# Kernel tuning notes

Hardware: AMD Instinct MI355X
Metric: run time of the kernel (lower is better)

The kernel has to match this reference:

```python
import jax, jax.numpy as jnp
import numpy as np

N = 100000       # nodes
E = 1000000      # edges
IN = 128         # in_dim
HID = 64         # hid_dim
NET = 4          # n_etypes
STEPS = 5        # n_steps
G = 128          # graphs in batch
LBL = 10         # num_labels


def setup_inputs() -> dict:
    key = jax.random.key(0)
    ks = jax.random.split(key, 20)
    def w(k, shape, fan_in):
        return jax.random.normal(k, shape, jnp.float32) / np.sqrt(fan_in)
    return dict(
        x=jax.random.normal(ks[0], (N, IN), jnp.float32),
        src=jax.random.randint(ks[1], (E,), 0, N),
        dst=jax.random.randint(ks[2], (E,), 0, N),
        etype=jax.random.randint(ks[3], (E,), 0, NET),
        node2graph=jnp.sort(jax.random.randint(ks[4], (N,), 0, G)),
        # linear_in
        W_in=w(ks[5], (HID, IN), IN), b_in=jnp.zeros((HID,), jnp.float32),
        # per-edge-type linears [n_etypes, out, in]
        We=w(ks[6], (NET, HID, HID), HID), be=jnp.zeros((NET, HID), jnp.float32),
        # GRUCell (torch layout: rows = [r; z; n])
        W_ih=w(ks[7], (3 * HID, HID), HID), b_ih=jnp.zeros((3 * HID,), jnp.float32),
        W_hh=w(ks[8], (3 * HID, HID), HID), b_hh=jnp.zeros((3 * HID,), jnp.float32),
        # classifier
        W1=w(ks[9], (HID // 2, HID), HID), b1=jnp.zeros((HID // 2,), jnp.float32),
        W2=w(ks[10], (LBL, HID // 2), HID // 2), b2=jnp.zeros((LBL,), jnp.float32),
    )


def reference(x, W_in, b_in, We, be, W_ih, b_ih, W_hh, b_hh, W1, b1, W2, b2,
              src, dst, etype, node2graph):
    h = x @ W_in.T + b_in                                  # [N, HID]
    for _ in range(STEPS):
        # per-etype linear on node states: trans[e] = h @ We[e].T + be[e]
        trans = jnp.einsum('nd,efd->enf', h, We) + be[:, None, :]  # [NET, N, HID]
        msgs = trans[etype, src]                           # [E, HID] gather per edge
        a = jax.ops.segment_sum(msgs, dst, num_segments=N)  # scatter-add aggregation
        # GRUCell(a, h)
        gi = a @ W_ih.T + b_ih
        gh = h @ W_hh.T + b_hh
        ir, iz, i_n = jnp.split(gi, 3, axis=-1)
        hr, hz, h_n = jnp.split(gh, 3, axis=-1)
        r = jax.nn.sigmoid(ir + hr)
        z = jax.nn.sigmoid(iz + hz)
        n = jnp.tanh(i_n + r * h_n)
        h = (1.0 - z) * n + z * h
    # dgl.mean_nodes: per-graph mean of node states
    cnt = jnp.maximum(jax.ops.segment_sum(jnp.ones((N,), h.dtype), node2graph, num_segments=G), 1.0)
    hg = jax.ops.segment_sum(h, node2graph, num_segments=G) / cnt[:, None]  # [G, HID]
    return jax.nn.relu(hg @ W1.T + b1) @ W2.T + b2         # [G, LBL]
```

## Files before the change

kernel.cpp:

```cpp
#include <hip/hip_runtime.h>
#include <hip/hip_bf16.h>
#include <math.h>

#define N_NODES 100000
#define N_EDGES 1000000
#define IN_DIM 128
#define HID 64
#define NET 4
#define STEPS 5
#define G_GRAPHS 128
#define LBL 10
#define NGRP 6250
#define NGRP_PAD 6256
#define NBKT 1024
#define TILE_E 8192

typedef __attribute__((ext_vector_type(8))) short short8;
typedef __attribute__((ext_vector_type(4))) float f32x4;
typedef unsigned short ushort_t;

__device__ inline ushort_t f2bf(float v) {
    __hip_bfloat16 b = __float2bfloat16(v);
    return __builtin_bit_cast(ushort_t, b);
}
__device__ inline float bf2f(ushort_t u) {
    __hip_bfloat16 b = __builtin_bit_cast(__hip_bfloat16, u);
    return __bfloat162float(b);
}


__global__ void k_pack_bc(const float* __restrict__ We, ushort_t* __restrict__ BC) {
    int idx = blockIdx.x * blockDim.x + threadIdx.x;
    if (idx >= 24 * 4 * 64 * 8) return;
    int j = idx & 7, lane = (idx >> 3) & 63, ct = (idx >> 9) & 3, sl = idx >> 11;
    int g = lane >> 4, u = lane & 15;
    int p = sl >> 3, ks = sl & 7;
    int k = ks * 32 + g * 8 + j;
    int t = k >> 6, d = k & 63;
    int o = ct * 16 + u;
    float val = We[t * 4096 + o * 64 + d];
    ushort_t hi = f2bf(val);
    BC[idx] = (p < 2) ? hi : f2bf(val - bf2f(hi));
}

__global__ void k_pack_b2(const float* __restrict__ W_ih, const float* __restrict__ b_ih,
                          const float* __restrict__ W_hh, const float* __restrict__ b_hh,
                          ushort_t* __restrict__ B2, float* __restrict__ bg2) {
    int idx = blockIdx.x * blockDim.x + threadIdx.x;
    if (idx >= 12 * 16 * 4 * 16 * 8) return;
    int j = idx & 7, u = (idx >> 3) & 15, g = (idx >> 7) & 3, ct = (idx >> 9) & 15, s = idx >> 13;
    int m = ct * 16 + u;
    int q = m >> 6, gate = (m >> 4) & 3, c = q * 16 + (m & 15);
    int k = (s & 3) * 32 + g * 8 + j;
    float val;
    if (gate == 0)      { int jr = c;        val = (k < 64) ? W_ih[jr * 64 + k] : W_hh[jr * 64 + k - 64]; }
    else if (gate == 1) { int jr = 64 + c;   val = (k < 64) ? W_ih[jr * 64 + k] : W_hh[jr * 64 + k - 64]; }
    else if (gate == 2) { int jr = 128 + c;  val = (k < 64) ? W_ih[jr * 64 + k] : 0.f; }
    else                { int jr = 128 + c;  val = (k < 64) ? 0.f : W_hh[jr * 64 + k - 64]; }
    ushort_t hi = f2bf(val);
    B2[idx] = (s < 8) ? hi : f2bf(val - bf2f(hi));
    if (s == 0 && g == 0 && j == 0) {
        float bv;
        if (gate == 0)      bv = b_ih[c] + b_hh[c];
        else if (gate == 1) bv = b_ih[64 + c] + b_hh[64 + c];
        else if (gate == 2) bv = b_ih[128 + c];
        else                bv = b_hh[128 + c];
        bg2[m] = bv;
    }
}

__global__ void k_pack_bin(const float* __restrict__ W_in, ushort_t* __restrict__ BIN) {
    int idx = blockIdx.x * blockDim.x + threadIdx.x;
    if (idx >= 24576) return;
    int j = idx & 7, lu = (idx >> 3) & 63, ct = (idx >> 9) & 3, s = idx >> 11;
    int g = lu >> 4, u = lu & 15;
    int m = ct * 16 + u;
    int k = (s & 3) * 32 + g * 8 + j;
    float val = W_in[m * 128 + k];
    ushort_t hi = f2bf(val);
    BIN[idx] = (s < 8) ? hi : f2bf(val - bf2f(hi));
}

__global__ __launch_bounds__(256) void k_linear_in(const float* __restrict__ x,
        const ushort_t* __restrict__ BIN, const float* __restrict__ b_in,
        ushort_t* __restrict__ AH, ushort_t* __restrict__ hrow) {
    __shared__ float hlds[4][16 * 68];
    int tid = threadIdx.x;
    int lane = tid & 63, wp = tid >> 6;
    int g = lane >> 4, u = lane & 15;
    int grp = blockIdx.x * 4 + wp;
    bool ok = grp < NGRP;
    int row = ok ? (grp * 16 + u) : 0;
    short8 xhi[4], xlo[4];
    #pragma unroll
    for (int ks = 0; ks < 4; ++ks) {
        const float* xp = &x[(size_t)row * 128 + ks * 32 + g * 8];
        float4 v0 = ok ? *(const float4*)xp : make_float4(0.f, 0.f, 0.f, 0.f);
        float4 v1 = ok ? *(const float4*)(xp + 4) : make_float4(0.f, 0.f, 0.f, 0.f);
        float vv[8] = {v0.x, v0.y, v0.z, v0.w, v1.x, v1.y, v1.z, v1.w};
        #pragma unroll
        for (int j = 0; j < 8; ++j) {
            ushort_t hh = f2bf(vv[j]);
            xhi[ks][j] = (short)hh;
            xlo[ks][j] = (short)f2bf(vv[j] - bf2f(hh));
        }
    }
    f32x4 zero = {0.f, 0.f, 0.f, 0.f};
    f32x4 acc[4] = {zero, zero, zero, zero};
    #pragma unroll
    for (int s = 0; s < 12; ++s) {
        int ks = s & 3;
        short8 af = (s < 4) ? xhi[ks] : (s < 8) ? xlo[ks] : xhi[ks];
        #pragma unroll
        for (int ct = 0; ct < 4; ++ct) {
            short8 bf = *(const short8*)&BIN[((size_t)(s * 4 + ct) * 64 + lane) * 8];
            acc[ct] = __builtin_amdgcn_mfma_f32_16x16x32_bf16(af, bf, acc[ct], 0, 0, 0);
        }
    }
    #pragma unroll
    for (int ct = 0; ct < 4; ++ct) {
        float bo = b_in[ct * 16 + u];
        #pragma unroll
        for (int j = 0; j < 4; ++j)
            hlds[wp][(g * 4 + j) * 68 + ct * 16 + u] = acc[ct][j] + bo;
    }
    __syncthreads();
    #pragma unroll
    for (int k = 0; k < 4; ++k) {
        int bi = g + 4 * k;
        short8 ov;
        #pragma unroll
        for (int j = 0; j < 8; ++j) {
            float v = hlds[wp][u * 68 + (bi & 7) * 8 + j];
            ushort_t hh = f2bf(v);
            ov[j] = (bi < 8) ? (short)hh : (short)f2bf(v - bf2f(hh));
        }
        int blk = (bi < 8) ? (8 + bi) : (24 + (bi - 8));
        if (ok) {
            *(short8*)&AH[((size_t)grp * 32 + blk) * 128 + u * 8] = ov;
            if (bi < 8)
                *(short8*)&hrow[((size_t)(grp * 16 + u)) * 64 + bi * 8] = ov;
        }
    }
}

__global__ __launch_bounds__(256) void k_bhist(const int* __restrict__ dst,
        int* __restrict__ bhist) {
    __shared__ int h[NBKT];
    for (int i = threadIdx.x; i < NBKT; i += 256) h[i] = 0;
    __syncthreads();
    int idx = blockIdx.x * 256 + threadIdx.x;
    for (int e = idx; e < N_EDGES; e += 256 * 256) atomicAdd(&h[dst[e] >> 7], 1);
    __syncthreads();
    for (int i = threadIdx.x; i < NBKT; i += 256) {
        int c = h[i];
        if (c) atomicAdd(&bhist[i], c);
    }
}

__global__ __launch_bounds__(1024) void k_bscan(const int* __restrict__ bhist,
        int* __restrict__ bbase, int* __restrict__ bcursor) {
    __shared__ int ts[NBKT];
    int t = threadIdx.x;
    int v = bhist[t];
    ts[t] = v;
    __syncthreads();
    for (int off = 1; off < NBKT; off <<= 1) {
        int u = (t >= off) ? ts[t - off] : 0;
        __syncthreads();
        ts[t] += u;
        __syncthreads();
    }
    int excl = ts[t] - v;
    bbase[t] = excl;
    bcursor[t] = excl;
    if (t == NBKT - 1) bbase[NBKT] = ts[NBKT - 1];
}

__global__ __launch_bounds__(512) void k_bscatter(const int* __restrict__ src,
        const int* __restrict__ dst, const int* __restrict__ et,
        int* __restrict__ bcursor, unsigned int* __restrict__ ebuf) {
    __shared__ int hcnt[NBKT], loff[NBKT], gpos[NBKT], ps[512];
    __shared__ unsigned int stage[TILE_E];
    __shared__ unsigned short sbkt[TILE_E];
    int tid = threadIdx.x;
    int base = blockIdx.x * TILE_E;
    int tilecnt = min(TILE_E, N_EDGES - base);
    for (int i = tid; i < NBKT; i += 512) hcnt[i] = 0;
    __syncthreads();
    #pragma unroll
    for (int k = 0; k < TILE_E / 512; ++k) {
        int e = base + tid + k * 512;
        if (e < N_EDGES) atomicAdd(&hcnt[dst[e] >> 7], 1);
    }
    __syncthreads();
    int c0 = hcnt[tid * 2], c1 = hcnt[tid * 2 + 1];
    ps[tid] = c0 + c1;
    __syncthreads();
    for (int off = 1; off < 512; off <<= 1) {
        int u = (tid >= off) ? ps[tid - off] : 0;
        __syncthreads();
        ps[tid] += u;
        __syncthreads();
    }
    int ex = ps[tid] - (c0 + c1);
    loff[tid * 2] = ex;
    loff[tid * 2 + 1] = ex + c0;
    for (int b = tid; b < NBKT; b += 512) {
        int c = hcnt[b];
        gpos[b] = c ? atomicAdd(&bcursor[b], c) : 0;
    }
    __syncthreads();
    for (int i = tid; i < NBKT; i += 512) hcnt[i] = 0;
    __syncthreads();
    #pragma unroll
    for (int k = 0; k < TILE_E / 512; ++k) {
        int e = base + tid + k * 512;
        if (e < N_EDGES) {
            int d = dst[e];
            int b = d >> 7;
            int r = atomicAdd(&hcnt[b], 1);
            int lp = loff[b] + r;
            stage[lp] = (unsigned int)src[e] | ((unsigned int)et[e] << 20)
                      | ((unsigned int)(d & 127) << 22);
            sbkt[lp] = (unsigned short)b;
        }
    }
    __syncthreads();
    for (int i = tid; i < tilecnt; i += 512) {
        int b = sbkt[i];
        ebuf[gpos[b] + (i - loff[b])] = stage[i];
    }
}

__global__ __launch_bounds__(256) void k_bcsr(const unsigned int* __restrict__ ebuf,
        const int* __restrict__ bbase, int* __restrict__ adj, int* __restrict__ row_ptr) {
    __shared__ int ncnt[128], noff[129], nps[128];
    int b = blockIdx.x;
    int tid = threadIdx.x;
    int ebeg = bbase[b], eend = bbase[b + 1];
    int ecnt = eend - ebeg;
    if (tid < 128) ncnt[tid] = 0;
    __syncthreads();
    for (int i = tid; i < ecnt; i += 256) atomicAdd(&ncnt[(ebuf[ebeg + i] >> 22) & 127], 1);
    __syncthreads();
    int v = (tid < 128) ? ncnt[tid] : 0;
    if (tid < 128) nps[tid] = v;
    __syncthreads();
    for (int off = 1; off < 128; off <<= 1) {
        int u = (tid >= off && tid < 128) ? nps[tid - off] : 0;
        __syncthreads();
        if (tid < 128) nps[tid] += u;
        __syncthreads();
    }
    if (tid < 128) noff[tid] = nps[tid] - v;
    if (tid == 127) noff[128] = nps[127];
    __syncthreads();
    if (tid < 128) ncnt[tid] = 0;
    __syncthreads();
    for (int i = tid; i < ecnt; i += 256) {
        unsigned int p = ebuf[ebeg + i];
        int nl = (p >> 22) & 127;
        int r = atomicAdd(&ncnt[nl], 1);
        adj[ebeg + noff[nl] + r] = (int)(p & 0x3FFFFF);
    }
    for (int i = tid; i <= 128; i += 256) {
        int n = b * 128 + i;
        if (n <= N_NODES) row_ptr[n] = ebeg + noff[i];
    }
}

__global__ __launch_bounds__(512) void k_step(const int* __restrict__ row_ptr,
        const int* __restrict__ adj, const ushort_t* __restrict__ hin,
        ushort_t* __restrict__ hout, ushort_t* __restrict__ AH,
        const ushort_t* __restrict__ BC, const float* __restrict__ be,
        const ushort_t* __restrict__ B2, const float* __restrict__ bg2) {
    __shared__ float smem[16896];
    float* aggf = smem;
    float* cnts = smem + 16640;
    ushort_t* als  = (ushort_t*)smem;
    ushort_t* hlds = (ushort_t*)((char*)smem + 17408);

    int tid = threadIdx.x, lane = tid & 63, wp = tid >> 6;
    int g = lane >> 4, u = lane & 15;
    int grp0 = blockIdx.x * 4;
    int nbase = grp0 * 16;

    #pragma unroll 1
    for (int r = 0; r < 8; ++r) {
        int nl = wp * 8 + r;
        int n = nbase + nl;
        float a0 = 0.f, a1 = 0.f, a2 = 0.f, a3 = 0.f;
        float c0 = 0.f, c1 = 0.f, c2 = 0.f, c3 = 0.f;
        if (n < N_NODES) {
            int beg = row_ptr[n], end = row_ptr[n + 1];
            int i = beg;
            for (; i + 4 <= end; i += 4) {
                int p0 = adj[i], p1 = adj[i + 1], p2 = adj[i + 2], p3 = adj[i + 3];
                float v0 = bf2f(hin[(size_t)(p0 & 0xFFFFF) * 64 + lane]);
                float v1 = bf2f(hin[(size_t)(p1 & 0xFFFFF) * 64 + lane]);
                float v2 = bf2f(hin[(size_t)(p2 & 0xFFFFF) * 64 + lane]);
                float v3 = bf2f(hin[(size_t)(p3 & 0xFFFFF) * 64 + lane]);
                int e0 = p0 >> 20, e1 = p1 >> 20, e2 = p2 >> 20, e3 = p3 >> 20;
                a0 += (e0 == 0) ? v0 : 0.f; a1 += (e0 == 1) ? v0 : 0.f;
                a2 += (e0 == 2) ? v0 : 0.f; a3 += (e0 == 3) ? v0 : 0.f;
                a0 += (e1 == 0) ? v1 : 0.f; a1 += (e1 == 1) ? v1 : 0.f;
                a2 += (e1 == 2) ? v1 : 0.f; a3 += (e1 == 3) ? v1 : 0.f;
                a0 += (e2 == 0) ? v2 : 0.f; a1 += (e2 == 1) ? v2 : 0.f;
                a2 += (e2 == 2) ? v2 : 0.f; a3 += (e2 == 3) ? v2 : 0.f;
                a0 += (e3 == 0) ? v3 : 0.f; a1 += (e3 == 1) ? v3 : 0.f;
                a2 += (e3 == 2) ? v3 : 0.f; a3 += (e3 == 3) ? v3 : 0.f;
                c0 += ((e0 == 0) ? 1.f : 0.f) + ((e1 == 0) ? 1.f : 0.f) + ((e2 == 0) ? 1.f : 0.f) + ((e3 == 0) ? 1.f : 0.f);
                c1 += ((e0 == 1) ? 1.f : 0.f) + ((e1 == 1) ? 1.f : 0.f) + ((e2 == 1) ? 1.f : 0.f) + ((e3 == 1) ? 1.f : 0.f);
                c2 += ((e0 == 2) ? 1.f : 0.f) + ((e1 == 2) ? 1.f : 0.f) + ((e2 == 2) ? 1.f : 0.f) + ((e3 == 2) ? 1.f : 0.f);
                c3 += ((e0 == 3) ? 1.f : 0.f) + ((e1 == 3) ? 1.f : 0.f) + ((e2 == 3) ? 1.f : 0.f) + ((e3 == 3) ? 1.f : 0.f);
            }
            for (; i < end; ++i) {
                int pk = adj[i];
                float v = bf2f(hin[(size_t)(pk & 0xFFFFF) * 64 + lane]);
                int e = pk >> 20;
                a0 += (e == 0) ? v : 0.f; a1 += (e == 1) ? v : 0.f;
                a2 += (e == 2) ? v : 0.f; a3 += (e == 3) ? v : 0.f;
                c0 += (e == 0) ? 1.f : 0.f; c1 += (e == 1) ? 1.f : 0.f;
                c2 += (e == 2) ? 1.f : 0.f; c3 += (e == 3) ? 1.f : 0.f;
            }
        }
        aggf[nl * 260 +   0 + lane] = a0;
        aggf[nl * 260 +  64 + lane] = a1;
        aggf[nl * 260 + 128 + lane] = a2;
        aggf[nl * 260 + 192 + lane] = a3;
        if (lane == 0) {
            cnts[nl * 4 + 0] = c0; cnts[nl * 4 + 1] = c1;
            cnts[nl * 4 + 2] = c2; cnts[nl * 4 + 3] = c3;
        }
    }
    __syncthreads();

    int rp1 = wp >> 1, cq = wp & 1;
    f32x4 zero = {0.f, 0.f, 0.f, 0.f};
    f32x4 acc1[2] = {zero, zero};
    #pragma unroll
    for (int ks = 0; ks < 8; ++ks) {
        const float* ap = &aggf[(rp1 * 16 + u) * 260 + ks * 32 + g * 8];
        f32x4 x0 = *(const f32x4*)ap;
        f32x4 x1 = *(const f32x4*)(ap + 4);
        short8 ahi, alo;
        #pragma unroll
        for (int j = 0; j < 4; ++j) {
            ushort_t hh = f2bf(x0[j]);
            ahi[j] = (short)hh; alo[j] = (short)f2bf(x0[j] - bf2f(hh));
            ushort_t hh2 = f2bf(x1[j]);
            ahi[4 + j] = (short)hh2; alo[4 + j] = (short)f2bf(x1[j] - bf2f(hh2));
        }
        #pragma unroll
        for (int p = 0; p < 3; ++p) {
            short8 af = (p == 1) ? alo : ahi;
            #pragma unroll
            for (int ct = 0; ct < 2; ++ct) {
                short8 bf = *(const short8*)&BC[((size_t)((p * 8 + ks) * 4 + cq * 2 + ct) * 64 + lane) * 8];
                acc1[ct] = __builtin_amdgcn_mfma_f32_16x16x32_bf16(af, bf, acc1[ct], 0, 0, 0);
            }
        }
    }
    __syncthreads();

    {
        float beL[2][4];
        #pragma unroll
        for (int ct = 0; ct < 2; ++ct)
            #pragma unroll
            for (int t = 0; t < 4; ++t)
                beL[ct][t] = be[t * 64 + cq * 32 + ct * 16 + u];
        #pragma unroll
        for (int j = 0; j < 4; ++j) {
            int row = rp1 * 16 + g * 4 + j;
            f32x4 cn = *(const f32x4*)&cnts[row * 4];
            #pragma unroll
            for (int ct = 0; ct < 2; ++ct) {
                float v = acc1[ct][j] + cn[0] * beL[ct][0] + cn[1] * beL[ct][1]
                                      + cn[2] * beL[ct][2] + cn[3] * beL[ct][3];
                int col = cq * 32 + ct * 16 + u;
                ushort_t hh = f2bf(v);
                als[row * 136 + col] = hh;
                als[row * 136 + 64 + col] = f2bf(v - bf2f(hh));
            }
        }
    }
    #pragma unroll
    for (int it = 0; it < 2; ++it) {
        int c = it * 512 + tid;
        int gl = c >> 8, r = c & 255, bi = r >> 4, uu = r & 15;
        int blk = (bi < 8) ? (8 + bi) : (24 + (bi - 8));
        *(short8*)&hlds[((gl * 16 + bi) * 16 + uu) * 8] =
            *(const short8*)&AH[((size_t)(grp0 + gl) * 32 + blk) * 128 + uu * 8];
    }
    __syncthreads();

    int q = wp & 3, rp2 = wp >> 2;
    f32x4 acc2[2][4];
    #pragma unroll
    for (int i = 0; i < 2; ++i)
        #pragma unroll
        for (int j = 0; j < 4; ++j) acc2[i][j] = zero;
    #pragma unroll
    for (int s = 0; s < 12; ++s) {
        int p2 = s >> 2, ks2 = s & 3;
        short8 bfr[4], afr[2];
        #pragma unroll
        for (int ct = 0; ct < 4; ++ct)
            bfr[ct] = *(const short8*)&B2[((size_t)(s * 16 + q * 4 + ct) * 64 + g * 16 + u) * 8];
        #pragma unroll
        for (int rt = 0; rt < 2; ++rt) {
            int row = rp2 * 32 + rt * 16 + u;
            if (ks2 < 2) {
                int base = ((p2 == 1) ? 64 : 0) + ks2 * 32 + g * 8;
                afr[rt] = *(const short8*)&als[row * 136 + base];
            } else {
                int part = (p2 == 1) ? 1 : 0;
                int gl = rp2 * 2 + rt;
                int bi = part * 8 + (ks2 - 2) * 4 + g;
                afr[rt] = *(const short8*)&hlds[((gl * 16 + bi) * 16 + u) * 8];
            }
        }
        #pragma unroll
        for (int rt = 0; rt < 2; ++rt)
            #pragma unroll
            for (int ct = 0; ct < 4; ++ct)
                acc2[rt][ct] = __builtin_amdgcn_mfma_f32_16x16x32_bf16(afr[rt], bfr[ct], acc2[rt][ct], 0, 0, 0);
    }
    __syncthreads();

    {
        float bgv[4];
        #pragma unroll
        for (int ct = 0; ct < 4; ++ct) bgv[ct] = bg2[q * 64 + ct * 16 + u];
        int hid = q * 16 + u;
        #pragma unroll
        for (int rt = 0; rt < 2; ++rt) {
            int gl = rp2 * 2 + rt;
            #pragma unroll
            for (int j = 0; j < 4; ++j) {
                int uu = g * 4 + j;
                int shi = ((gl * 16 + (hid >> 3)) * 16 + uu) * 8 + (hid & 7);
                int slo = ((gl * 16 + 8 + (hid >> 3)) * 16 + uu) * 8 + (hid & 7);
                float ho = bf2f(hlds[shi]) + bf2f(hlds[slo]);
                float rs  = acc2[rt][0][j] + bgv[0];
                float zs  = acc2[rt][1][j] + bgv[1];
                float inn = acc2[rt][2][j] + bgv[2];
                float hnn = acc2[rt][3][j] + bgv[3];
                float rr = 1.f / (1.f + __expf(-rs));
                float zz = 1.f / (1.f + __expf(-zs));
                float t = inn + rr * hnn;
                float e2 = __expf(2.f * t);
                float nn = 1.f - 2.f / (e2 + 1.f);
                float hnew = (1.f - zz) * nn + zz * ho;
                ushort_t hh = f2bf(hnew);
                hlds[shi] = hh;
                hlds[slo] = f2bf(hnew - bf2f(hh));
            }
        }
    }
    __syncthreads();

    #pragma unroll
    for (int it = 0; it < 2; ++it) {
        int c = it * 512 + tid;
        int gl = c >> 8, r = c & 255, bi = r >> 4, uu = r & 15;
        short8 v = *(const short8*)&hlds[((gl * 16 + bi) * 16 + uu) * 8];
        int blk = (bi < 8) ? (8 + bi) : (24 + (bi - 8));
        *(short8*)&AH[((size_t)(grp0 + gl) * 32 + blk) * 128 + uu * 8] = v;
        if (bi < 8)
            *(short8*)&hout[((size_t)((grp0 + gl) * 16 + uu)) * 64 + bi * 8] = v;
    }
}

__global__ __launch_bounds__(256) void k_pool(const int* __restrict__ n2g,
        const ushort_t* __restrict__ AH, float* __restrict__ hg) {
    int gidx = blockIdx.x;
    int lo = 0, hi = N_NODES;
    while (lo < hi) { int mid = (lo + hi) >> 1; if (n2g[mid] < gidx) lo = mid + 1; else hi = mid; }
    int s = lo;
    hi = N_NODES;
    while (lo < hi) { int mid = (lo + hi) >> 1; if (n2g[mid] < gidx + 1) lo = mid + 1; else hi = mid; }
    int e = lo;
    int w = threadIdx.x >> 6, lane = threadIdx.x & 63;
    int bh = 8 + (lane >> 3), bl = 24 + (lane >> 3), el = lane & 7;
    float sum = 0.f;
    for (int n = s + w; n < e; n += 4) {
        size_t base = (size_t)(n >> 4) * 4096 + (size_t)(n & 15) * 8;
        sum += bf2f(AH[base + bh * 128 + el]) + bf2f(AH[base + bl * 128 + el]);
    }
    __shared__ float red[4][64];
    red[w][lane] = sum;
    __syncthreads();
    if (threadIdx.x < 64) {
        float tot = red[0][lane] + red[1][lane] + red[2][lane] + red[3][lane];
        float cnt = (float)(e - s);
        hg[gidx * 64 + lane] = tot / fmaxf(cnt, 1.f);
    }
}

__global__ __launch_bounds__(64) void k_cls(const float* __restrict__ hg,
        const float* __restrict__ W1, const float* __restrict__ b1,
        const float* __restrict__ W2, const float* __restrict__ b2,
        float* __restrict__ out) {
    int gidx = blockIdx.x;
    __shared__ float v[64];
    __shared__ float m[32];
    v[threadIdx.x] = hg[gidx * 64 + threadIdx.x];
    __syncthreads();
    if (threadIdx.x < 32) {
        float a = b1[threadIdx.x];
        #pragma unroll 8
        for (int k = 0; k < 64; ++k) a = fmaf(v[k], W1[threadIdx.x * 64 + k], a);
        m[threadIdx.x] = fmaxf(a, 0.f);
    }
    __syncthreads();
    if (threadIdx.x < 10) {
        float a = b2[threadIdx.x];
        #pragma unroll
        for (int j = 0; j < 32; ++j) a = fmaf(m[j], W2[threadIdx.x * 32 + j], a);
        out[gidx * 10 + threadIdx.x] = a;
    }
}

extern "C" void kernel_launch(void* const* d_in, const int* in_sizes, int n_in,
                              void* d_out, int out_size, void* d_ws, size_t ws_size,
                              hipStream_t stream) {
    const float* x    = (const float*)d_in[0];
    const int* src    = (const int*)d_in[1];
    const int* dst    = (const int*)d_in[2];
    const int* etype  = (const int*)d_in[3];
    const int* n2g    = (const int*)d_in[4];
    const float* W_in = (const float*)d_in[5];
    const float* b_in = (const float*)d_in[6];
    const float* We   = (const float*)d_in[7];
    const float* be   = (const float*)d_in[8];
    const float* W_ih = (const float*)d_in[9];
    const float* b_ih = (const float*)d_in[10];
    const float* W_hh = (const float*)d_in[11];
    const float* b_hh = (const float*)d_in[12];
    const float* W1   = (const float*)d_in[13];
    const float* b1   = (const float*)d_in[14];
    const float* W2   = (const float*)d_in[15];
    const float* b2   = (const float*)d_in[16];
    float* out = (float*)d_out;

    char* wsb = (char*)d_ws;
    size_t off = 0;
    auto alloc = [&](size_t bytes) -> void* {
        void* p = wsb + off;
        off += (bytes + 255) & ~(size_t)255;
        return p;
    };
    ushort_t* AH      = (ushort_t*)alloc((size_t)NGRP_PAD * 4096 * 2);
    ushort_t* hrowA   = (ushort_t*)alloc((size_t)NGRP_PAD * 16 * 64 * 2);
    ushort_t* hrowB   = (ushort_t*)alloc((size_t)NGRP_PAD * 16 * 64 * 2);
    int*      adj     = (int*)     alloc((size_t)N_EDGES * 4);
    unsigned int* ebuf = (unsigned int*)alloc((size_t)N_EDGES * 4);
    int*      row_ptr = (int*)     alloc((size_t)(N_NODES + 1) * 4);
    int*      bhist   = (int*)     alloc((size_t)NBKT * 4);
    int*      bbase   = (int*)     alloc((size_t)(NBKT + 1) * 4);
    int*      bcursor = (int*)     alloc((size_t)NBKT * 4);
    ushort_t* B2      = (ushort_t*)alloc((size_t)12 * 16 * 4 * 16 * 8 * 2);
    float*    bg2     = (float*)   alloc(256 * 4);
    ushort_t* BIN     = (ushort_t*)alloc((size_t)24576 * 2);
    ushort_t* BC      = (ushort_t*)alloc((size_t)24 * 4 * 64 * 8 * 2);
    float*    hg      = (float*)   alloc(128 * 64 * 4);

    hipMemsetAsync(AH + (size_t)NGRP * 4096, 0, (size_t)(NGRP_PAD - NGRP) * 4096 * 2, stream);

    hipLaunchKernelGGL(k_pack_b2, dim3(384), dim3(256), 0, stream, W_ih, b_ih, W_hh, b_hh, B2, bg2);
    hipLaunchKernelGGL(k_pack_bin, dim3(96), dim3(256), 0, stream, W_in, BIN);
    hipLaunchKernelGGL(k_pack_bc, dim3(192), dim3(256), 0, stream, We, BC);
    hipLaunchKernelGGL(k_linear_in, dim3((NGRP + 3) / 4), dim3(256), 0, stream, x, BIN, b_in, AH, hrowA);

    hipMemsetAsync(bhist, 0, (size_t)NBKT * 4, stream);
    hipLaunchKernelGGL(k_bhist, dim3(256), dim3(256), 0, stream, dst, bhist);
    hipLaunchKernelGGL(k_bscan, dim3(1), dim3(1024), 0, stream, bhist, bbase, bcursor);
    hipLaunchKernelGGL(k_bscatter, dim3((N_EDGES + TILE_E - 1) / TILE_E), dim3(512), 0, stream,
                       src, dst, etype, bcursor, ebuf);
    hipLaunchKernelGGL(k_bcsr, dim3(NBKT), dim3(256), 0, stream, ebuf, bbase, adj, row_ptr);

    int sblk = NGRP_PAD / 4;
    for (int step = 0; step < STEPS; ++step) {
        const ushort_t* hin = (step & 1) ? hrowB : hrowA;
        ushort_t* hout      = (step & 1) ? hrowA : hrowB;
        hipLaunchKernelGGL(k_step, dim3(sblk), dim3(512), 0, stream,
                           row_ptr, adj, hin, hout, AH, BC, be, B2, bg2);
    }
    hipLaunchKernelGGL(k_pool, dim3(G_GRAPHS), dim3(256), 0, stream, n2g, AH, hg);
    hipLaunchKernelGGL(k_cls, dim3(G_GRAPHS), dim3(64), 0, stream, hg, W1, b1, W2, b2, out);
}
```

Before: 841.4 us.

## Sort CSR edges by (dst, etype) and halve k_step tile to 32 nodes

The CSR build now buckets edges by destination node and edge type, producing a four-way row pointer per node. The gather loop can then sum each edge-type segment directly, with no per-edge select over four accumulators, and counts come from pointer differences. Separately, each k_step block now handles 32 nodes instead of 64, halving shared memory and doubling the block count for more occupancy, at the cost of fewer MFMAs per B-fragment load. The padded buffers and the memset are removed because 6250 groups divide evenly by 2.

```diff
diff --git a/kernel.cpp b/kernel.cpp
--- a/kernel.cpp
+++ b/kernel.cpp
@@ -11,7 +11,6 @@
 #define G_GRAPHS 128
 #define LBL 10
 #define NGRP 6250
-#define NGRP_PAD 6256
 #define NBKT 1024
 #define TILE_E 8192
 
@@ -234,111 +233,97 @@
 }
 
 __global__ __launch_bounds__(256) void k_bcsr(const unsigned int* __restrict__ ebuf,
-        const int* __restrict__ bbase, int* __restrict__ adj, int* __restrict__ row_ptr) {
-    __shared__ int ncnt[128], noff[129], nps[128];
+        const int* __restrict__ bbase, int* __restrict__ adj, int* __restrict__ row_ptr2) {
+    __shared__ int ncnt[512], noff[513], ps[256];
     int b = blockIdx.x;
     int tid = threadIdx.x;
     int ebeg = bbase[b], eend = bbase[b + 1];
     int ecnt = eend - ebeg;
-    if (tid < 128) ncnt[tid] = 0;
-    __syncthreads();
-    for (int i = tid; i < ecnt; i += 256) atomicAdd(&ncnt[(ebuf[ebeg + i] >> 22) & 127], 1);
-    __syncthreads();
-    int v = (tid < 128) ? ncnt[tid] : 0;
-    if (tid < 128) nps[tid] = v;
-    __syncthreads();
-    for (int off = 1; off < 128; off <<= 1) {
-        int u = (tid >= off && tid < 128) ? nps[tid - off] : 0;
-        __syncthreads();
-        if (tid < 128) nps[tid] += u;
-        __syncthreads();
-    }
-    if (tid < 128) noff[tid] = nps[tid] - v;
-    if (tid == 127) noff[128] = nps[127];
-    __syncthreads();
-    if (tid < 128) ncnt[tid] = 0;
+    ncnt[tid] = 0; ncnt[tid + 256] = 0;
     __syncthreads();
     for (int i = tid; i < ecnt; i += 256) {
         unsigned int p = ebuf[ebeg + i];
-        int nl = (p >> 22) & 127;
-        int r = atomicAdd(&ncnt[nl], 1);
-        adj[ebeg + noff[nl] + r] = (int)(p & 0x3FFFFF);
-    }
-    for (int i = tid; i <= 128; i += 256) {
-        int n = b * 128 + i;
-        if (n <= N_NODES) row_ptr[n] = ebeg + noff[i];
-    }
-}
-
-__global__ __launch_bounds__(512) void k_step(const int* __restrict__ row_ptr,
+        int key = (int)((((p >> 22) & 127) << 2) | ((p >> 20) & 3));
+        atomicAdd(&ncnt[key], 1);
+    }
+    __syncthreads();
+    int c0 = ncnt[2 * tid], c1 = ncnt[2 * tid + 1];
+    ps[tid] = c0 + c1;
+    __syncthreads();
+    for (int off = 1; off < 256; off <<= 1) {
+        int u = (tid >= off) ? ps[tid - off] : 0;
+        __syncthreads();
+        ps[tid] += u;
+        __syncthreads();
+    }
+    int ex = ps[tid] - (c0 + c1);
+    noff[2 * tid] = ex;
+    noff[2 * tid + 1] = ex + c0;
+    if (tid == 255) noff[512] = ps[255];
+    __syncthreads();
+    ncnt[tid] = 0; ncnt[tid + 256] = 0;
+    __syncthreads();
+    for (int i = tid; i < ecnt; i += 256) {
+        unsigned int p = ebuf[ebeg + i];
+        int key = (int)((((p >> 22) & 127) << 2) | ((p >> 20) & 3));
+        int r = atomicAdd(&ncnt[key], 1);
+        adj[ebeg + noff[key] + r] = (int)(p & 0xFFFFF);
+    }
+    for (int k = tid; k < 512; k += 256)
+        row_ptr2[b * 512 + k] = ebeg + noff[k];
+    if (b == NBKT - 1 && tid == 0) row_ptr2[NBKT * 512] = eend;
+}
+
+__global__ __launch_bounds__(512) void k_step(const int* __restrict__ row_ptr2,
         const int* __restrict__ adj, const ushort_t* __restrict__ hin,
         ushort_t* __restrict__ hout, ushort_t* __restrict__ AH,
         const ushort_t* __restrict__ BC, const float* __restrict__ be,
         const ushort_t* __restrict__ B2, const float* __restrict__ bg2) {
-    __shared__ float smem[16896];
+    __shared__ float smem[8448];
     float* aggf = smem;
-    float* cnts = smem + 16640;
+    float* cnts = smem + 8320;
     ushort_t* als  = (ushort_t*)smem;
-    ushort_t* hlds = (ushort_t*)((char*)smem + 17408);
+    ushort_t* hlds = (ushort_t*)((char*)smem + 9216);
 
     int tid = threadIdx.x, lane = tid & 63, wp = tid >> 6;
     int g = lane >> 4, u = lane & 15;
-    int grp0 = blockIdx.x * 4;
+    int grp0 = blockIdx.x * 2;
     int nbase = grp0 * 16;
 
     #pragma unroll 1
-    for (int r = 0; r < 8; ++r) {
-        int nl = wp * 8 + r;
+    for (int r = 0; r < 4; ++r) {
+        int nl = wp * 4 + r;
         int n = nbase + nl;
-        float a0 = 0.f, a1 = 0.f, a2 = 0.f, a3 = 0.f;
-        float c0 = 0.f, c1 = 0.f, c2 = 0.f, c3 = 0.f;
-        if (n < N_NODES) {
-            int beg = row_ptr[n], end = row_ptr[n + 1];
-            int i = beg;
-            for (; i + 4 <= end; i += 4) {
-                int p0 = adj[i], p1 = adj[i + 1], p2 = adj[i + 2], p3 = adj[i + 3];
-                float v0 = bf2f(hin[(size_t)(p0 & 0xFFFFF) * 64 + lane]);
-                float v1 = bf2f(hin[(size_t)(p1 & 0xFFFFF) * 64 + lane]);
-                float v2 = bf2f(hin[(size_t)(p2 & 0xFFFFF) * 64 + lane]);
-                float v3 = bf2f(hin[(size_t)(p3 & 0xFFFFF) * 64 + lane]);
-                int e0 = p0 >> 20, e1 = p1 >> 20, e2 = p2 >> 20, e3 = p3 >> 20;
-                a0 += (e0 == 0) ? v0 : 0.f; a1 += (e0 == 1) ? v0 : 0.f;
-                a2 += (e0 == 2) ? v0 : 0.f; a3 += (e0 == 3) ? v0 : 0.f;
-                a0 += (e1 == 0) ? v1 : 0.f; a1 += (e1 == 1) ? v1 : 0.f;
-                a2 += (e1 == 2) ? v1 : 0.f; a3 += (e1 == 3) ? v1 : 0.f;
-                a0 += (e2 == 0) ? v2 : 0.f; a1 += (e2 == 1) ? v2 : 0.f;
-                a2 += (e2 == 2) ? v2 : 0.f; a3 += (e2 == 3) ? v2 : 0.f;
-                a0 += (e3 == 0) ? v3 : 0.f; a1 += (e3 == 1) ? v3 : 0.f;
-                a2 += (e3 == 2) ? v3 : 0.f; a3 += (e3 == 3) ? v3 : 0.f;
-                c0 += ((e0 == 0) ? 1.f : 0.f) + ((e1 == 0) ? 1.f : 0.f) + ((e2 == 0) ? 1.f : 0.f) + ((e3 == 0) ? 1.f : 0.f);
-                c1 += ((e0 == 1) ? 1.f : 0.f) + ((e1 == 1) ? 1.f : 0.f) + ((e2 == 1) ? 1.f : 0.f) + ((e3 == 1) ? 1.f : 0.f);
-                c2 += ((e0 == 2) ? 1.f : 0.f) + ((e1 == 2) ? 1.f : 0.f) + ((e2 == 2) ? 1.f : 0.f) + ((e3 == 2) ? 1.f : 0.f);
-                c3 += ((e0 == 3) ? 1.f : 0.f) + ((e1 == 3) ? 1.f : 0.f) + ((e2 == 3) ? 1.f : 0.f) + ((e3 == 3) ? 1.f : 0.f);
+        const int* op = &row_ptr2[(size_t)n * 4];
+        int o0 = op[0], o1 = op[1], o2 = op[2], o3 = op[3], o4 = op[4];
+        #pragma unroll
+        for (int t = 0; t < 4; ++t) {
+            int i = (t == 0) ? o0 : (t == 1) ? o1 : (t == 2) ? o2 : o3;
+            int e = (t == 0) ? o1 : (t == 1) ? o2 : (t == 2) ? o3 : o4;
+            float s0 = 0.f, s1 = 0.f, s2 = 0.f, s3 = 0.f;
+            for (; i + 4 <= e; i += 4) {
+                int a0 = adj[i], a1 = adj[i + 1], a2 = adj[i + 2], a3 = adj[i + 3];
+                s0 += bf2f(hin[(size_t)a0 * 64 + lane]);
+                s1 += bf2f(hin[(size_t)a1 * 64 + lane]);
+                s2 += bf2f(hin[(size_t)a2 * 64 + lane]);
+                s3 += bf2f(hin[(size_t)a3 * 64 + lane]);
             }
-            for (; i < end; ++i) {
-                int pk = adj[i];
-                float v = bf2f(hin[(size_t)(pk & 0xFFFFF) * 64 + lane]);
-                int e = pk >> 20;
-                a0 += (e == 0) ? v : 0.f; a1 += (e == 1) ? v : 0.f;
-                a2 += (e == 2) ? v : 0.f; a3 += (e == 3) ? v : 0.f;
-                c0 += (e == 0) ? 1.f : 0.f; c1 += (e == 1) ? 1.f : 0.f;
-                c2 += (e == 2) ? 1.f : 0.f; c3 += (e == 3) ? 1.f : 0.f;
-            }
-        }
-        aggf[nl * 260 +   0 + lane] = a0;
-        aggf[nl * 260 +  64 + lane] = a1;
-        aggf[nl * 260 + 128 + lane] = a2;
-        aggf[nl * 260 + 192 + lane] = a3;
+            for (; i < e; ++i)
+                s0 += bf2f(hin[(size_t)adj[i] * 64 + lane]);
+            aggf[nl * 260 + t * 64 + lane] = (s0 + s1) + (s2 + s3);
+        }
         if (lane == 0) {
-            cnts[nl * 4 + 0] = c0; cnts[nl * 4 + 1] = c1;
-            cnts[nl * 4 + 2] = c2; cnts[nl * 4 + 3] = c3;
-        }
-    }
-    __syncthreads();
-
-    int rp1 = wp >> 1, cq = wp & 1;
+            cnts[nl * 4 + 0] = (float)(o1 - o0);
+            cnts[nl * 4 + 1] = (float)(o2 - o1);
+            cnts[nl * 4 + 2] = (float)(o3 - o2);
+            cnts[nl * 4 + 3] = (float)(o4 - o3);
+        }
+    }
+    __syncthreads();
+
+    int rp1 = wp >> 2, cq = wp & 3;
     f32x4 zero = {0.f, 0.f, 0.f, 0.f};
-    f32x4 acc1[2] = {zero, zero};
+    f32x4 acc1 = zero;
     #pragma unroll
     for (int ks = 0; ks < 8; ++ks) {
         const float* ap = &aggf[(rp1 * 16 + u) * 260 + ks * 32 + g * 8];
@@ -355,41 +340,31 @@
         #pragma unroll
         for (int p = 0; p < 3; ++p) {
             short8 af = (p == 1) ? alo : ahi;
-            #pragma unroll
-            for (int ct = 0; ct < 2; ++ct) {
-                short8 bf = *(const short8*)&BC[((size_t)((p * 8 + ks) * 4 + cq * 2 + ct) * 64 + lane) * 8];
-                acc1[ct] = __builtin_amdgcn_mfma_f32_16x16x32_bf16(af, bf, acc1[ct], 0, 0, 0);
-            }
+            short8 bf = *(const short8*)&BC[((size_t)((p * 8 + ks) * 4 + cq) * 64 + lane) * 8];
+            acc1 = __builtin_amdgcn_mfma_f32_16x16x32_bf16(af, bf, acc1, 0, 0, 0);
         }
     }
     __syncthreads();
 
     {
-        float beL[2][4];
-        #pragma unroll
-        for (int ct = 0; ct < 2; ++ct)
-            #pragma unroll
-            for (int t = 0; t < 4; ++t)
-                beL[ct][t] = be[t * 64 + cq * 32 + ct * 16 + u];
+        float beL[4];
+        #pragma unroll
+        for (int t = 0; t < 4; ++t) beL[t] = be[t * 64 + cq * 16 + u];
         #pragma unroll
         for (int j = 0; j < 4; ++j) {
             int row = rp1 * 16 + g * 4 + j;
             f32x4 cn = *(const f32x4*)&cnts[row * 4];
-            #pragma unroll
-            for (int ct = 0; ct < 2; ++ct) {
-                float v = acc1[ct][j] + cn[0] * beL[ct][0] + cn[1] * beL[ct][1]
-                                      + cn[2] * beL[ct][2] + cn[3] * beL[ct][3];
-                int col = cq * 32 + ct * 16 + u;
-                ushort_t hh = f2bf(v);
-                als[row * 136 + col] = hh;
-                als[row * 136 + 64 + col] = f2bf(v - bf2f(hh));
-            }
-        }
-    }
-    #pragma unroll
-    for (int it = 0; it < 2; ++it) {
-        int c = it * 512 + tid;
-        int gl = c >> 8, r = c & 255, bi = r >> 4, uu = r & 15;
+            float v = acc1[j] + cn[0] * beL[0] + cn[1] * beL[1]
+                              + cn[2] * beL[2] + cn[3] * beL[3];
+            int col = cq * 16 + u;
+            ushort_t hh = f2bf(v);
+            als[row * 136 + col] = hh;
+            als[row * 136 + 64 + col] = f2bf(v - bf2f(hh));
+        }
+    }
+    {
+        int c = tid;
+        int gl = c >> 8, rr = c & 255, bi = rr >> 4, uu = rr & 15;
         int blk = (bi < 8) ? (8 + bi) : (24 + (bi - 8));
         *(short8*)&hlds[((gl * 16 + bi) * 16 + uu) * 8] =
             *(const short8*)&AH[((size_t)(grp0 + gl) * 32 + blk) * 128 + uu * 8];
@@ -397,36 +372,24 @@
     __syncthreads();
 
     int q = wp & 3, rp2 = wp >> 2;
-    f32x4 acc2[2][4];
-    #pragma unroll
-    for (int i = 0; i < 2; ++i)
-        #pragma unroll
-        for (int j = 0; j < 4; ++j) acc2[i][j] = zero;
+    f32x4 acc2[4] = {zero, zero, zero, zero};
     #pragma unroll
     for (int s = 0; s < 12; ++s) {
         int p2 = s >> 2, ks2 = s & 3;
-        short8 bfr[4], afr[2];
-        #pragma unroll
-        for (int ct = 0; ct < 4; ++ct)
-            bfr[ct] = *(const short8*)&B2[((size_t)(s * 16 + q * 4 + ct) * 64 + g * 16 + u) * 8];
-        #pragma unroll
-        for (int rt = 0; rt < 2; ++rt) {
-            int row = rp2 * 32 + rt * 16 + u;
-            if (ks2 < 2) {
-                int base = ((p2 == 1) ? 64 : 0) + ks2 * 32 + g * 8;
-                afr[rt] = *(const short8*)&als[row * 136 + base];
-            } else {
-                int part = (p2 == 1) ? 1 : 0;
-                int gl = rp2 * 2 + rt;
-                int bi = part * 8 + (ks2 - 2) * 4 + g;
-                afr[rt] = *(const short8*)&hlds[((gl * 16 + bi) * 16 + u) * 8];
-            }
-        }
-        #pragma unroll
-        for (int rt = 0; rt < 2; ++rt)
-            #pragma unroll
-            for (int ct = 0; ct < 4; ++ct)
-                acc2[rt][ct] = __builtin_amdgcn_mfma_f32_16x16x32_bf16(afr[rt], bfr[ct], acc2[rt][ct], 0, 0, 0);
+        short8 afr;
+        if (ks2 < 2) {
+            int base = ((p2 == 1) ? 64 : 0) + ks2 * 32 + g * 8;
+            afr = *(const short8*)&als[(rp2 * 16 + u) * 136 + base];
+        } else {
+            int part = (p2 == 1) ? 1 : 0;
+            int bi = part * 8 + (ks2 - 2) * 4 + g;
+            afr = *(const short8*)&hlds[((rp2 * 16 + bi) * 16 + u) * 8];
+        }
+        #pragma unroll
+        for (int ct = 0; ct < 4; ++ct) {
+            short8 bfr = *(const short8*)&B2[((size_t)(s * 16 + q * 4 + ct) * 64 + g * 16 + u) * 8];
+            acc2[ct] = __builtin_amdgcn_mfma_f32_16x16x32_bf16(afr, bfr, acc2[ct], 0, 0, 0);
+        }
     }
     __syncthreads();
 
@@ -436,36 +399,31 @@
         for (int ct = 0; ct < 4; ++ct) bgv[ct] = bg2[q * 64 + ct * 16 + u];
         int hid = q * 16 + u;
         #pragma unroll
-        for (int rt = 0; rt < 2; ++rt) {
-            int gl = rp2 * 2 + rt;
-            #pragma unroll
-            for (int j = 0; j < 4; ++j) {
-                int uu = g * 4 + j;
-                int shi = ((gl * 16 + (hid >> 3)) * 16 + uu) * 8 + (hid & 7);
-                int slo = ((gl * 16 + 8 + (hid >> 3)) * 16 + uu) * 8 + (hid & 7);
-                float ho = bf2f(hlds[shi]) + bf2f(hlds[slo]);
-                float rs  = acc2[rt][0][j] + bgv[0];
-                float zs  = acc2[rt][1][j] + bgv[1];
-                float inn = acc2[rt][2][j] + bgv[2];
-                float hnn = acc2[rt][3][j] + bgv[3];
-                float rr = 1.f / (1.f + __expf(-rs));
-                float zz = 1.f / (1.f + __expf(-zs));
-                float t = inn + rr * hnn;
-                float e2 = __expf(2.f * t);
-                float nn = 1.f - 2.f / (e2 + 1.f);
-                float hnew = (1.f - zz) * nn + zz * ho;
-                ushort_t hh = f2bf(hnew);
-                hlds[shi] = hh;
-                hlds[slo] = f2bf(hnew - bf2f(hh));
-            }
-        }
-    }
-    __syncthreads();
-
-    #pragma unroll
-    for (int it = 0; it < 2; ++it) {
-        int c = it * 512 + tid;
-        int gl = c >> 8, r = c & 255, bi = r >> 4, uu = r & 15;
+        for (int j = 0; j < 4; ++j) {
+            int uu = g * 4 + j;
+            int shi = ((rp2 * 16 + (hid >> 3)) * 16 + uu) * 8 + (hid & 7);
+            int slo = ((rp2 * 16 + 8 + (hid >> 3)) * 16 + uu) * 8 + (hid & 7);
+            float ho = bf2f(hlds[shi]) + bf2f(hlds[slo]);
+            float rs  = acc2[0][j] + bgv[0];
+            float zs  = acc2[1][j] + bgv[1];
+            float inn = acc2[2][j] + bgv[2];
+            float hnn = acc2[3][j] + bgv[3];
+            float rr = 1.f / (1.f + __expf(-rs));
+            float zz = 1.f / (1.f + __expf(-zs));
+            float t = inn + rr * hnn;
+            float e2 = __expf(2.f * t);
+            float nn = 1.f - 2.f / (e2 + 1.f);
+            float hnew = (1.f - zz) * nn + zz * ho;
+            ushort_t hh = f2bf(hnew);
+            hlds[shi] = hh;
+            hlds[slo] = f2bf(hnew - bf2f(hh));
+        }
+    }
+    __syncthreads();
+
+    {
+        int c = tid;
+        int gl = c >> 8, rr = c & 255, bi = rr >> 4, uu = rr & 15;
         short8 v = *(const short8*)&hlds[((gl * 16 + bi) * 16 + uu) * 8];
         int blk = (bi < 8) ? (8 + bi) : (24 + (bi - 8));
         *(short8*)&AH[((size_t)(grp0 + gl) * 32 + blk) * 128 + uu * 8] = v;
@@ -553,22 +511,20 @@
         off += (bytes + 255) & ~(size_t)255;
         return p;
     };
-    ushort_t* AH      = (ushort_t*)alloc((size_t)NGRP_PAD * 4096 * 2);
-    ushort_t* hrowA   = (ushort_t*)alloc((size_t)NGRP_PAD * 16 * 64 * 2);
-    ushort_t* hrowB   = (ushort_t*)alloc((size_t)NGRP_PAD * 16 * 64 * 2);
-    int*      adj     = (int*)     alloc((size_t)N_EDGES * 4);
+    ushort_t* AH       = (ushort_t*)alloc((size_t)NGRP * 4096 * 2);
+    ushort_t* hrowA    = (ushort_t*)alloc((size_t)N_NODES * 64 * 2);
+    ushort_t* hrowB    = (ushort_t*)alloc((size_t)N_NODES * 64 * 2);
+    int*      adj      = (int*)     alloc((size_t)N_EDGES * 4);
     unsigned int* ebuf = (unsigned int*)alloc((size_t)N_EDGES * 4);
-    int*      row_ptr = (int*)     alloc((size_t)(N_NODES + 1) * 4);
-    int*      bhist   = (int*)     alloc((size_t)NBKT * 4);
-    int*      bbase   = (int*)     alloc((size_t)(NBKT + 1) * 4);
-    int*      bcursor = (int*)     alloc((size_t)NBKT * 4);
-    ushort_t* B2      = (ushort_t*)alloc((size_t)12 * 16 * 4 * 16 * 8 * 2);
-    float*    bg2     = (float*)   alloc(256 * 4);
-    ushort_t* BIN     = (ushort_t*)alloc((size_t)24576 * 2);
-    ushort_t* BC      = (ushort_t*)alloc((size_t)24 * 4 * 64 * 8 * 2);
-    float*    hg      = (float*)   alloc(128 * 64 * 4);
-
-    hipMemsetAsync(AH + (size_t)NGRP * 4096, 0, (size_t)(NGRP_PAD - NGRP) * 4096 * 2, stream);
+    int*      row_ptr2 = (int*)     alloc(((size_t)NBKT * 512 + 1) * 4);
+    int*      bhist    = (int*)     alloc((size_t)NBKT * 4);
+    int*      bbase    = (int*)     alloc((size_t)(NBKT + 1) * 4);
+    int*      bcursor  = (int*)     alloc((size_t)NBKT * 4);
+    ushort_t* B2       = (ushort_t*)alloc((size_t)12 * 16 * 4 * 16 * 8 * 2);
+    float*    bg2      = (float*)   alloc(256 * 4);
+    ushort_t* BIN      = (ushort_t*)alloc((size_t)24576 * 2);
+    ushort_t* BC       = (ushort_t*)alloc((size_t)24 * 4 * 64 * 8 * 2);
+    float*    hg       = (float*)   alloc(128 * 64 * 4);
 
     hipLaunchKernelGGL(k_pack_b2, dim3(384), dim3(256), 0, stream, W_ih, b_ih, W_hh, b_hh, B2, bg2);
     hipLaunchKernelGGL(k_pack_bin, dim3(96), dim3(256), 0, stream, W_in, BIN);
@@ -580,14 +536,14 @@
     hipLaunchKernelGGL(k_bscan, dim3(1), dim3(1024), 0, stream, bhist, bbase, bcursor);
     hipLaunchKernelGGL(k_bscatter, dim3((N_EDGES + TILE_E - 1) / TILE_E), dim3(512), 0, stream,
                        src, dst, etype, bcursor, ebuf);
-    hipLaunchKernelGGL(k_bcsr, dim3(NBKT), dim3(256), 0, stream, ebuf, bbase, adj, row_ptr);
-
-    int sblk = NGRP_PAD / 4;
+    hipLaunchKernelGGL(k_bcsr, dim3(NBKT), dim3(256), 0, stream, ebuf, bbase, adj, row_ptr2);
+
+    int sblk = NGRP / 2;
     for (int step = 0; step < STEPS; ++step) {
         const ushort_t* hin = (step & 1) ? hrowB : hrowA;
         ushort_t* hout      = (step & 1) ? hrowA : hrowB;
         hipLaunchKernelGGL(k_step, dim3(sblk), dim3(512), 0, stream,
-                           row_ptr, adj, hin, hout, AH, BC, be, B2, bg2);
+                           row_ptr2, adj, hin, hout, AH, BC, be, B2, bg2);
     }
     hipLaunchKernelGGL(k_pool, dim3(G_GRAPHS), dim3(256), 0, stream, n2g, AH, hg);
     hipLaunchKernelGGL(k_cls, dim3(G_GRAPHS), dim3(64), 0, stream, hg, W1, b1, W2, b2, out);
```

After: 825.6 us. Within noise of the previous version (-1.9%).
